# Kernel optimization log

Measured on AMD Instinct MI355X. Metric: run time of the kernel, lower is better.

## Reference

```python
import jax, jax.numpy as jnp
import numpy as np

B, T, INPUT_DIM, Z_DIM, RNN_DIM = 512, 200, 88, 100, 60


def setup_inputs() -> dict:
    key = jax.random.key(0)
    ks = jax.random.split(key, 18)
    sd = 0.05
    return {
        "mini_batch": jax.random.normal(ks[0], (B, T, INPUT_DIM), jnp.float32),
        "mini_batch_reversed": jax.random.normal(ks[1], (B, T, INPUT_DIM), jnp.float32),
        "mini_batch_mask": jnp.ones((B, T), jnp.float32),
        "mini_batch_seq_lengths": jax.random.randint(ks[2], (B,), T // 2, T + 1),
        "eps": jax.random.normal(ks[3], (T, B, Z_DIM), jnp.float32),
        # RNN (relu, 1 layer) params
        "W_ih": jax.random.normal(ks[4], (RNN_DIM, INPUT_DIM), jnp.float32) * sd,
        "W_hh": jax.random.normal(ks[5], (RNN_DIM, RNN_DIM), jnp.float32) * sd,
        "b_ih": jnp.zeros((RNN_DIM,), jnp.float32),
        "b_hh": jnp.zeros((RNN_DIM,), jnp.float32),
        "h_0": jax.random.normal(ks[6], (RNN_DIM,), jnp.float32),
        "z_q_0": jnp.zeros((Z_DIM,), jnp.float32),
        # Combiner params
        "W_zh": jax.random.normal(ks[7], (RNN_DIM, Z_DIM), jnp.float32) * sd,
        "b_zh": jnp.zeros((RNN_DIM,), jnp.float32),
        "W_hl": jax.random.normal(ks[8], (Z_DIM, RNN_DIM), jnp.float32) * sd,
        "b_hl": jnp.zeros((Z_DIM,), jnp.float32),
        "W_hs": jax.random.normal(ks[9], (Z_DIM, RNN_DIM), jnp.float32) * sd,
        "b_hs": jnp.zeros((Z_DIM,), jnp.float32),
    }


def _encoder(mini_batch_reversed, seq_lengths, eps,
             W_ih, W_hh, b_ih, b_hh, h_0, z_q_0,
             W_zh, b_zh, W_hl, b_hl, W_hs, b_hs):
    Bn = mini_batch_reversed.shape[0]
    Tn = mini_batch_reversed.shape[1]

    # --- relu RNN over reversed input, batch_first -> scan over time ---
    xs = jnp.transpose(mini_batch_reversed, (1, 0, 2))  # [T, B, input_dim]
    h0 = jnp.broadcast_to(h_0, (Bn, RNN_DIM))

    def rnn_step(h, x_t):
        h = jax.nn.relu(x_t @ W_ih.T + b_ih + h @ W_hh.T + b_hh)
        return h, h

    _, rnn_out = jax.lax.scan(rnn_step, h0, xs)          # [T, B, rnn_dim]
    rnn_out = jnp.transpose(rnn_out, (1, 0, 2))          # [B, T, rnn_dim]

    # --- pad_and_reverse: reverse each sequence by its length, zero-pad tail ---
    t_idx = jnp.arange(Tn)
    rev_idx = seq_lengths[:, None] - 1 - t_idx[None, :]  # [B, T]
    valid = rev_idx >= 0
    gathered = jnp.take_along_axis(rnn_out, jnp.clip(rev_idx, 0)[:, :, None], axis=1)
    rnn_rev = jnp.where(valid[:, :, None], gathered, 0.0)  # [B, T, rnn_dim]

    # --- sequential combiner + reparameterized sampling ---
    h_seq = jnp.transpose(rnn_rev, (1, 0, 2))            # [T, B, rnn_dim]
    z0 = jnp.broadcast_to(z_q_0, (Bn, Z_DIM))

    def comb_step(z_prev, inp):
        h_t, eps_t = inp
        h_comb = 0.5 * (jnp.tanh(z_prev @ W_zh.T + b_zh) + h_t)
        loc = h_comb @ W_hl.T + b_hl
        scale = jax.nn.softplus(h_comb @ W_hs.T + b_hs)
        z_t = loc + scale * eps_t
        return z_t, (z_t, loc, scale)

    _, (zs, locs, scales) = jax.lax.scan(comb_step, z0, (h_seq, eps))
    # [T, B, z] -> [B, T, z]
    tr = lambda a: jnp.transpose(a, (1, 0, 2))
    return tr(zs), tr(locs), tr(scales)


def reference(mini_batch, mini_batch_reversed, mini_batch_mask,
              mini_batch_seq_lengths, eps,
              W_ih, W_hh, b_ih, b_hh, h_0, z_q_0,
              W_zh, b_zh, W_hl, b_hl, W_hs, b_hs):
    return _encoder(mini_batch_reversed, mini_batch_seq_lengths, eps,
                    W_ih, W_hh, b_ih, b_hh, h_0, z_q_0,
                    W_zh, b_zh, W_hl, b_hl, W_hs, b_hs)
```

## Files before the change

kernel.cpp:

```cpp
#include <hip/hip_runtime.h>
#include <cmath>

#define NB 512
#define NT 200
#define NIN 88
#define NH 60
#define NZ 100

typedef float f2 __attribute__((ext_vector_type(2)));
typedef _Float16 h2v __attribute__((ext_vector_type(2)));
typedef _Float16 h8v __attribute__((ext_vector_type(8)));

__device__ __forceinline__ f2 pk_fma(f2 a, f2 b, f2 c) {
    return __builtin_elementwise_fma(a, b, c);
}
__device__ __forceinline__ float dot2(h2v a, h2v b, float c) {
#if __has_builtin(__builtin_amdgcn_fdot2)
    return __builtin_amdgcn_fdot2(a, b, c, false);
#else
    return fmaf((float)a.x, (float)b.x, fmaf((float)a.y, (float)b.y, c));
#endif
}
__device__ __forceinline__ float fast_tanh(float x) {
    float cx = fminf(fmaxf(x, -10.f), 10.f);
    float e  = __expf(2.f * cx);
    return (e - 1.f) * __builtin_amdgcn_rcpf(e + 1.f);
}
__device__ __forceinline__ float fast_softplus(float x) {
    return fmaxf(x, 0.f) + __logf(1.f + __expf(-fabsf(x)));
}
__device__ __forceinline__ void block_sync_lds() {
    asm volatile("s_waitcnt lgkmcnt(0)" ::: "memory");
    __builtin_amdgcn_s_barrier();
    asm volatile("" ::: "memory");
}

#define TCHUNKS 5
#define TCL (NT / TCHUNKS)

__global__ __launch_bounds__(128, 1)
void pre_kernel(const float* __restrict__ xrev, const float* __restrict__ W_ih,
                const float* __restrict__ b_ih, const float* __restrict__ b_hh,
                float* __restrict__ pre)
{
    __shared__ __align__(16) float xw[2][NIN];

    const int b    = blockIdx.x;
    const int tc   = blockIdx.y;
    const int wv   = threadIdx.x >> 6;
    const int lane = threadIdx.x & 63;

    f2 wih2[44];
    float bias = 0.f;
    if (lane < NH) {
        const float4* p = reinterpret_cast<const float4*>(W_ih + lane * NIN);
#pragma unroll
        for (int k = 0; k < 22; ++k) {
            float4 v = p[k];
            wih2[2*k]   = f2{v.x, v.y};
            wih2[2*k+1] = f2{v.z, v.w};
        }
        bias = b_ih[lane] + b_hh[lane];
    } else {
#pragma unroll
        for (int k = 0; k < 44; ++k) wih2[k] = f2{0.f, 0.f};
    }

    const float* xb = xrev + ((size_t)b * NT + (size_t)tc * TCL) * NIN;
    float* pb = pre + ((size_t)b * NT + (size_t)tc * TCL) * NH;

    float xa = xb[(size_t)wv * NIN + lane];
    float xc = (lane < NIN - 64) ? xb[(size_t)wv * NIN + 64 + lane] : 0.f;

    for (int k = 0; k < TCL / 2; ++k) {
        const int t = wv + 2 * k;
        xw[wv][lane] = xa;
        if (lane < NIN - 64) xw[wv][64 + lane] = xc;
        const int tn = t + 2;
        if (tn < TCL) {
            xa = xb[(size_t)tn * NIN + lane];
            xc = (lane < NIN - 64) ? xb[(size_t)tn * NIN + 64 + lane] : 0.f;
        }
        const float4* x4 = reinterpret_cast<const float4*>(xw[wv]);
        f2 a0 = f2{bias, 0.f}, a1 = f2{0.f, 0.f};
#pragma unroll
        for (int q = 0; q < 22; ++q) {
            float4 v = x4[q];
            a0 = pk_fma(f2{v.x, v.y}, wih2[2*q],   a0);
            a1 = pk_fma(f2{v.z, v.w}, wih2[2*q+1], a1);
        }
        if (lane < NH) pb[(size_t)t * NH + lane] = (a0.x + a1.x) + (a0.y + a1.y);
    }
}

__global__ __launch_bounds__(128, 1)
void fused128(const int*   __restrict__ seqlen,
              const float* __restrict__ eps,
              const float* __restrict__ W_hh,
              const float* __restrict__ h0,
              const float* __restrict__ zq0,
              const float* __restrict__ W_zh,
              const float* __restrict__ b_zh,
              const float* __restrict__ W_hl,
              const float* __restrict__ b_hl,
              const float* __restrict__ W_hs,
              const float* __restrict__ b_hs,
              const float* __restrict__ pre,
              float* __restrict__ out)
{
    __shared__ __align__(16) float    h_rev[NT][NH];
    __shared__ __align__(16) float    hbuf[NH + 4];
    __shared__ __align__(16) _Float16 zbh[2][112];
    __shared__ __align__(16) _Float16 hch[2][64];

    const int b    = blockIdx.x;
    const int tid  = threadIdx.x;
    const int wv   = tid >> 6;
    const int lane = tid & 63;
    const int sl   = seqlen[b];

    {
        const int tail = (NT - sl) * NH;
        float* base = &h_rev[0][0] + sl * NH;
        for (int i = tid; i < tail; i += 128) base[i] = 0.0f;
    }
    if (tid < 12) { zbh[0][100 + tid] = (_Float16)0; zbh[1][100 + tid] = (_Float16)0; }
    if (lane >= NH) hch[wv][lane] = (_Float16)0;

    f2  whh2[30];
    h2v wzh_h[52];
    h2v wl_h[32];
    h2v ws_h[32];
    float bz = 0.f, bl = 0.f, bs = 0.f;
    const int  o   = 50 * wv + lane;
    const bool oln = (lane < 50);
    float e_cur = 0.f;

    if (oln) {
        const float4* p = reinterpret_cast<const float4*>(W_hl + o * NH);
        const float4* q = reinterpret_cast<const float4*>(W_hs + o * NH);
#pragma unroll
        for (int k = 0; k < 15; ++k) {
            float4 v = p[k];
            wl_h[2*k]   = h2v{(_Float16)(0.5f * v.x), (_Float16)(0.5f * v.y)};
            wl_h[2*k+1] = h2v{(_Float16)(0.5f * v.z), (_Float16)(0.5f * v.w)};
            float4 u = q[k];
            ws_h[2*k]   = h2v{(_Float16)(0.5f * u.x), (_Float16)(0.5f * u.y)};
            ws_h[2*k+1] = h2v{(_Float16)(0.5f * u.z), (_Float16)(0.5f * u.w)};
        }
        wl_h[30] = h2v{(_Float16)0, (_Float16)0}; wl_h[31] = wl_h[30];
        ws_h[30] = wl_h[30]; ws_h[31] = wl_h[30];
        bl = b_hl[o];
        bs = b_hs[o];
        e_cur = eps[(size_t)b * NZ + o];
        zbh[0][o] = (_Float16)zq0[o];
    } else {
#pragma unroll
        for (int k = 0; k < 32; ++k) { wl_h[k] = h2v{(_Float16)0, (_Float16)0}; ws_h[k] = wl_h[k]; }
    }

    if (wv == 0) {
        if (lane < NH) {
            const float4* q = reinterpret_cast<const float4*>(W_hh + lane * NH);
#pragma unroll
            for (int k = 0; k < 15; ++k) {
                float4 v = q[k];
                whh2[2*k]   = f2{v.x, v.y};
                whh2[2*k+1] = f2{v.z, v.w};
            }
            hbuf[lane] = h0[lane];
        } else {
#pragma unroll
            for (int k = 0; k < 30; ++k) whh2[k] = f2{0.f, 0.f};
        }
    } else {
        if (lane < NH) {
            const float4* q = reinterpret_cast<const float4*>(W_zh + lane * NZ);
#pragma unroll
            for (int k = 0; k < 25; ++k) {
                float4 v = q[k];
                wzh_h[2*k]   = h2v{(_Float16)v.x, (_Float16)v.y};
                wzh_h[2*k+1] = h2v{(_Float16)v.z, (_Float16)v.w};
            }
            bz = b_zh[lane];
        } else {
#pragma unroll
            for (int k = 0; k < 50; ++k) wzh_h[k] = h2v{(_Float16)0, (_Float16)0};
        }
        wzh_h[50] = h2v{(_Float16)0, (_Float16)0};
        wzh_h[51] = wzh_h[50];
    }
    __syncthreads();

    if (wv == 0) {
        const float* pb = pre + (size_t)b * NT * NH;
        const bool hl = (lane < NH);
        float p0 = hl ? pb[0 * NH + lane] : 0.f;
        float p1 = hl ? pb[1 * NH + lane] : 0.f;
        float p2 = hl ? pb[2 * NH + lane] : 0.f;
        float p3 = hl ? pb[3 * NH + lane] : 0.f;
        for (int t = 0; t < NT; ++t) {
            float pn = (t + 4 < NT && hl) ? pb[(size_t)(t + 4) * NH + lane] : 0.f;
            const float4* h4 = reinterpret_cast<const float4*>(hbuf);
            f2 a0 = f2{p0, 0.f}, a1 = f2{0.f, 0.f};
#pragma unroll
            for (int k = 0; k < 15; ++k) {
                float4 v = h4[k];
                a0 = pk_fma(f2{v.x, v.y}, whh2[2*k],   a0);
                a1 = pk_fma(f2{v.z, v.w}, whh2[2*k+1], a1);
            }
            float hn = fmaxf((a0.x + a1.x) + (a0.y + a1.y), 0.f);
            if (hl) {
                hbuf[lane] = hn;
                if (t < sl) h_rev[sl - 1 - t][lane] = hn;
            }
            p0 = p1; p1 = p2; p2 = p3; p3 = pn;
        }
        if (lane < NH) {
            const float4* q = reinterpret_cast<const float4*>(W_zh + lane * NZ);
#pragma unroll
            for (int k = 0; k < 25; ++k) {
                float4 v = q[k];
                wzh_h[2*k]   = h2v{(_Float16)v.x, (_Float16)v.y};
                wzh_h[2*k+1] = h2v{(_Float16)v.z, (_Float16)v.w};
            }
            bz = b_zh[lane];
        } else {
#pragma unroll
            for (int k = 0; k < 50; ++k) wzh_h[k] = h2v{(_Float16)0, (_Float16)0};
        }
        wzh_h[50] = h2v{(_Float16)0, (_Float16)0};
        wzh_h[51] = wzh_h[50];
    }
    block_sync_lds();

    float* out_z = out;
    float* out_l = out + (size_t)NB * NT * NZ;
    float* out_s = out + (size_t)2 * NB * NT * NZ;

    for (int t = 0; t < NT; ++t) {
        const int r = t & 1;

        float hrow = (lane < NH) ? h_rev[t][lane] : 0.f;

        const h8v* z8 = reinterpret_cast<const h8v*>(&zbh[r][0]);
        float za0 = 0.f, za1 = 0.f, za2 = 0.f, za3 = 0.f;
#pragma unroll
        for (int k = 0; k < 13; ++k) {
            h8v v = z8[k];
            za0 = dot2(h2v{v[0], v[1]}, wzh_h[4*k+0], za0);
            za1 = dot2(h2v{v[2], v[3]}, wzh_h[4*k+1], za1);
            za2 = dot2(h2v{v[4], v[5]}, wzh_h[4*k+2], za2);
            za3 = dot2(h2v{v[6], v[7]}, wzh_h[4*k+3], za3);
        }

        float e_nxt = (oln && t + 1 < NT)
                      ? eps[((size_t)(t + 1) * NB + b) * NZ + o] : 0.f;

        if (lane < NH) {
            float a = (za0 + za1) + (za2 + za3) + bz;
            hch[wv][lane] = (_Float16)(fast_tanh(a) + hrow);
        }

        const h8v* h8p = reinterpret_cast<const h8v*>(&hch[wv][0]);
        float l0 = 0.f, l1 = 0.f, l2 = 0.f, l3 = 0.f;
        float s0 = 0.f, s1 = 0.f, s2 = 0.f, s3 = 0.f;
#pragma unroll
        for (int k = 0; k < 8; ++k) {
            h8v v = h8p[k];
            h2v x0 = h2v{v[0], v[1]}, x1 = h2v{v[2], v[3]};
            h2v x2 = h2v{v[4], v[5]}, x3 = h2v{v[6], v[7]};
            l0 = dot2(x0, wl_h[4*k+0], l0);
            l1 = dot2(x1, wl_h[4*k+1], l1);
            l2 = dot2(x2, wl_h[4*k+2], l2);
            l3 = dot2(x3, wl_h[4*k+3], l3);
            s0 = dot2(x0, ws_h[4*k+0], s0);
            s1 = dot2(x1, ws_h[4*k+1], s1);
            s2 = dot2(x2, ws_h[4*k+2], s2);
            s3 = dot2(x3, ws_h[4*k+3], s3);
        }
        if (oln) {
            float loc = (l0 + l1) + (l2 + l3) + bl;
            float ps  = (s0 + s1) + (s2 + s3) + bs;
            float sc  = fast_softplus(ps);
            float zv  = loc + sc * e_cur;
            size_t oi = ((size_t)b * NT + t) * NZ + o;
            out_z[oi] = zv;
            out_l[oi] = loc;
            out_s[oi] = sc;
            zbh[r ^ 1][o] = (_Float16)zv;
            e_cur = e_nxt;
        }
        block_sync_lds();
    }
}

__global__ __launch_bounds__(128, 1)
void encoder_mono(const float* __restrict__ xrev, const int* __restrict__ seqlen,
                  const float* __restrict__ eps,
                  const float* __restrict__ W_ih, const float* __restrict__ W_hh,
                  const float* __restrict__ b_ih, const float* __restrict__ b_hh,
                  const float* __restrict__ h0,   const float* __restrict__ zq0,
                  const float* __restrict__ W_zh, const float* __restrict__ b_zh,
                  const float* __restrict__ W_hl, const float* __restrict__ b_hl,
                  const float* __restrict__ W_hs, const float* __restrict__ b_hs,
                  float* __restrict__ out)
{
    __shared__ __align__(16) float h_rev[NT][NH];
    __shared__ __align__(16) float xbuf[NIN];
    __shared__ __align__(16) float hbuf[NH];
    __shared__ __align__(16) float zbuf[NZ];
    __shared__ __align__(16) float hcomb[NH];

    const int b = blockIdx.x, tid = threadIdx.x;
    const int wave = tid >> 6, lane = tid & 63;
    const int sl = seqlen[b];

    for (int i = tid; i < NT * NH; i += 128) (&h_rev[0][0])[i] = 0.0f;
    __syncthreads();

    if (wave == 0) {
        float wih[NIN], whh[NH];
        float bias = 0.f;
        if (lane < NH) {
            const float4* pp = reinterpret_cast<const float4*>(W_ih + lane * NIN);
#pragma unroll
            for (int k = 0; k < NIN / 4; ++k) {
                float4 v = pp[k];
                wih[4*k+0]=v.x; wih[4*k+1]=v.y; wih[4*k+2]=v.z; wih[4*k+3]=v.w;
            }
            const float4* q = reinterpret_cast<const float4*>(W_hh + lane * NH);
#pragma unroll
            for (int k = 0; k < NH / 4; ++k) {
                float4 v = q[k];
                whh[4*k+0]=v.x; whh[4*k+1]=v.y; whh[4*k+2]=v.z; whh[4*k+3]=v.w;
            }
            bias = b_ih[lane] + b_hh[lane];
            hbuf[lane] = h0[lane];
        } else {
#pragma unroll
            for (int k = 0; k < NIN; ++k) wih[k] = 0.f;
#pragma unroll
            for (int k = 0; k < NH; ++k) whh[k] = 0.f;
        }
        const float* xb = xrev + (size_t)b * NT * NIN;
        float xa = xb[lane];
        float xc = (lane < NIN - 64) ? xb[64 + lane] : 0.f;
        for (int t = 0; t < NT; ++t) {
            xbuf[lane] = xa;
            if (lane < NIN - 64) xbuf[64 + lane] = xc;
            if (t + 1 < NT) {
                xa = xb[(size_t)(t+1)*NIN + lane];
                xc = (lane < NIN - 64) ? xb[(size_t)(t+1)*NIN + 64 + lane] : 0.f;
            }
            float a0=0.f,a1=0.f,a2=0.f,a3=0.f;
            const float4* x4 = reinterpret_cast<const float4*>(xbuf);
#pragma unroll
            for (int k = 0; k < NIN / 4; ++k) {
                float4 v = x4[k];
                a0 += v.x*wih[4*k+0]; a1 += v.y*wih[4*k+1];
                a2 += v.z*wih[4*k+2]; a3 += v.w*wih[4*k+3];
            }
            const float4* h4 = reinterpret_cast<const float4*>(hbuf);
#pragma unroll
            for (int k = 0; k < NH / 4; ++k) {
                float4 v = h4[k];
                a0 += v.x*whh[4*k+0]; a1 += v.y*whh[4*k+1];
                a2 += v.z*whh[4*k+2]; a3 += v.w*whh[4*k+3];
            }
            float hn = fmaxf((a0+a1)+(a2+a3)+bias, 0.f);
            if (lane < NH) {
                hbuf[lane] = hn;
                if (t < sl) h_rev[sl-1-t][lane] = hn;
            }
        }
    }
    __syncthreads();

    const int o = 50 * wave + lane;
    float wzr[NZ]; float bz = 0.f;
    if (wave == 0 && lane < NH) {
        const float4* pp = reinterpret_cast<const float4*>(W_zh + lane * NZ);
#pragma unroll
        for (int k = 0; k < NZ / 4; ++k) {
            float4 v = pp[k];
            wzr[4*k+0]=v.x; wzr[4*k+1]=v.y; wzr[4*k+2]=v.z; wzr[4*k+3]=v.w;
        }
        bz = b_zh[lane];
    } else {
#pragma unroll
        for (int k = 0; k < NZ; ++k) wzr[k] = 0.f;
    }
    float wl[NH], ws_[NH]; float bl = 0.f, bs = 0.f;
    if (lane < 50) {
        const float4* pp = reinterpret_cast<const float4*>(W_hl + o * NH);
        const float4* q  = reinterpret_cast<const float4*>(W_hs + o * NH);
#pragma unroll
        for (int k = 0; k < NH / 4; ++k) {
            float4 v = pp[k];
            wl[4*k+0]=v.x; wl[4*k+1]=v.y; wl[4*k+2]=v.z; wl[4*k+3]=v.w;
            float4 u = q[k];
            ws_[4*k+0]=u.x; ws_[4*k+1]=u.y; ws_[4*k+2]=u.z; ws_[4*k+3]=u.w;
        }
        bl = b_hl[o]; bs = b_hs[o];
        zbuf[o] = zq0[o];
    } else {
#pragma unroll
        for (int k = 0; k < NH; ++k) { wl[k]=0.f; ws_[k]=0.f; }
    }
    __syncthreads();

    float* out_z = out;
    float* out_l = out + (size_t)NB * NT * NZ;
    float* out_s = out + (size_t)2 * NB * NT * NZ;
    const float* epsb = eps + (size_t)b * NZ;
    float e_cur = (lane < 50) ? epsb[o] : 0.f;

    for (int t = 0; t < NT; ++t) {
        if (wave == 0) {
            float a0=0.f,a1=0.f,a2=0.f,a3=0.f;
            const float4* z4 = reinterpret_cast<const float4*>(zbuf);
#pragma unroll
            for (int k = 0; k < NZ / 4; ++k) {
                float4 v = z4[k];
                a0 += v.x*wzr[4*k+0]; a1 += v.y*wzr[4*k+1];
                a2 += v.z*wzr[4*k+2]; a3 += v.w*wzr[4*k+3];
            }
            if (lane < NH) {
                float a = (a0+a1)+(a2+a3)+bz;
                hcomb[lane] = 0.5f * (fast_tanh(a) + h_rev[t][lane]);
            }
        }
        block_sync_lds();
        float e_nxt = 0.f;
        if (t + 1 < NT && lane < 50) e_nxt = epsb[(size_t)(t+1)*NB*NZ + o];
        if (lane < 50) {
            float c0=0.f,c1=0.f,c2=0.f,c3=0.f, d0=0.f,d1=0.f,d2=0.f,d3=0.f;
            const float4* h4 = reinterpret_cast<const float4*>(hcomb);
#pragma unroll
            for (int k = 0; k < NH / 4; ++k) {
                float4 v = h4[k];
                c0 += v.x*wl[4*k+0];  c1 += v.y*wl[4*k+1];
                c2 += v.z*wl[4*k+2];  c3 += v.w*wl[4*k+3];
                d0 += v.x*ws_[4*k+0]; d1 += v.y*ws_[4*k+1];
                d2 += v.z*ws_[4*k+2]; d3 += v.w*ws_[4*k+3];
            }
            float loc = (c0+c1)+(c2+c3)+bl;
            float ps  = (d0+d1)+(d2+d3)+bs;
            float sc  = fast_softplus(ps);
            float zv  = loc + sc * e_cur;
            size_t oi = ((size_t)b * NT + t) * NZ + o;
            out_z[oi]=zv; out_l[oi]=loc; out_s[oi]=sc;
            zbuf[o]=zv;
        }
        e_cur = e_nxt;
        block_sync_lds();
    }
}

extern "C" void kernel_launch(void* const* d_in, const int* in_sizes, int n_in,
                              void* d_out, int out_size, void* d_ws, size_t ws_size,
                              hipStream_t stream) {
    const float* xrev   = (const float*)d_in[1];
    const int*   seqlen = (const int*)  d_in[3];
    const float* eps    = (const float*)d_in[4];
    const float* W_ih   = (const float*)d_in[5];
    const float* W_hh   = (const float*)d_in[6];
    const float* b_ih   = (const float*)d_in[7];
    const float* b_hh   = (const float*)d_in[8];
    const float* h0     = (const float*)d_in[9];
    const float* zq0    = (const float*)d_in[10];
    const float* W_zh   = (const float*)d_in[11];
    const float* b_zh   = (const float*)d_in[12];
    const float* W_hl   = (const float*)d_in[13];
    const float* b_hl   = (const float*)d_in[14];
    const float* W_hs   = (const float*)d_in[15];
    const float* b_hs   = (const float*)d_in[16];
    float* out = (float*)d_out;

    const size_t pre_bytes = (size_t)NB * NT * NH * sizeof(float);
    if (ws_size >= pre_bytes) {
        float* pre = (float*)d_ws;
        pre_kernel<<<dim3(NB, TCHUNKS), 128, 0, stream>>>(xrev, W_ih, b_ih, b_hh, pre);
        fused128<<<NB, 128, 0, stream>>>(seqlen, eps, W_hh, h0, zq0,
                                         W_zh, b_zh, W_hl, b_hl, W_hs, b_hs,
                                         pre, out);
    } else {
        encoder_mono<<<NB, 128, 0, stream>>>(xrev, seqlen, eps,
                                             W_ih, W_hh, b_ih, b_hh, h0, zq0,
                                             W_zh, b_zh, W_hl, b_hl, W_hs, b_hs,
                                             out);
    }
}
```

Baseline: 311.8 us.

## Process one batch element per wavefront, removing block barriers in the recurrence loops

The fused kernel now gives each wavefront its own batch element, so a 128-thread block handles two elements and the grid is halved. Each wave runs both the RNN scan and the combiner scan itself, so the per-step block barrier and the cross-wave split of the output rows go away. Each lane now computes two outputs, and the reversed hidden states are kept in LDS as fp16. The costs are more registers per lane for the doubled weight sets, no overlap between the RNN phase and the combiner phase, and some extra precision loss on h. Correctness now depends on wavefront lockstep for the LDS handoffs that the removed barrier used to order.

```diff
diff --git a/kernel.cpp b/kernel.cpp
--- a/kernel.cpp
+++ b/kernel.cpp
@@ -94,72 +94,51 @@
 }
 
 __global__ __launch_bounds__(128, 1)
-void fused128(const int*   __restrict__ seqlen,
-              const float* __restrict__ eps,
-              const float* __restrict__ W_hh,
-              const float* __restrict__ h0,
-              const float* __restrict__ zq0,
-              const float* __restrict__ W_zh,
-              const float* __restrict__ b_zh,
-              const float* __restrict__ W_hl,
-              const float* __restrict__ b_hl,
-              const float* __restrict__ W_hs,
-              const float* __restrict__ b_hs,
-              const float* __restrict__ pre,
-              float* __restrict__ out)
+void fused1w(const int*   __restrict__ seqlen,
+             const float* __restrict__ eps,
+             const float* __restrict__ W_hh,
+             const float* __restrict__ h0,
+             const float* __restrict__ zq0,
+             const float* __restrict__ W_zh,
+             const float* __restrict__ b_zh,
+             const float* __restrict__ W_hl,
+             const float* __restrict__ b_hl,
+             const float* __restrict__ W_hs,
+             const float* __restrict__ b_hs,
+             const float* __restrict__ pre,
+             float* __restrict__ out)
 {
-    __shared__ __align__(16) float    h_rev[NT][NH];
-    __shared__ __align__(16) float    hbuf[NH + 4];
+    __shared__ __align__(16) _Float16 h_rev_h[2][NT][NH];
+    __shared__ __align__(16) float    hbuf[2][64];
     __shared__ __align__(16) _Float16 zbh[2][112];
     __shared__ __align__(16) _Float16 hch[2][64];
 
-    const int b    = blockIdx.x;
-    const int tid  = threadIdx.x;
-    const int wv   = tid >> 6;
-    const int lane = tid & 63;
+    const int wv   = threadIdx.x >> 6;
+    const int lane = threadIdx.x & 63;
+    const int b    = blockIdx.x * 2 + wv;
     const int sl   = seqlen[b];
 
     {
         const int tail = (NT - sl) * NH;
-        float* base = &h_rev[0][0] + sl * NH;
-        for (int i = tid; i < tail; i += 128) base[i] = 0.0f;
-    }
-    if (tid < 12) { zbh[0][100 + tid] = (_Float16)0; zbh[1][100 + tid] = (_Float16)0; }
+        _Float16* base = &h_rev_h[wv][sl][0];
+        for (int i = lane; i < tail; i += 64) base[i] = (_Float16)0;
+    }
+    if (lane < 12) zbh[wv][100 + lane] = (_Float16)0;
     if (lane >= NH) hch[wv][lane] = (_Float16)0;
 
-    f2  whh2[30];
-    h2v wzh_h[52];
-    h2v wl_h[32];
-    h2v ws_h[32];
-    float bz = 0.f, bl = 0.f, bs = 0.f;
-    const int  o   = 50 * wv + lane;
     const bool oln = (lane < 50);
-    float e_cur = 0.f;
-
+    const int  o1  = lane;
+    const int  o2  = lane + 50;
+    float e1 = 0.f, e2 = 0.f;
     if (oln) {
-        const float4* p = reinterpret_cast<const float4*>(W_hl + o * NH);
-        const float4* q = reinterpret_cast<const float4*>(W_hs + o * NH);
-#pragma unroll
-        for (int k = 0; k < 15; ++k) {
-            float4 v = p[k];
-            wl_h[2*k]   = h2v{(_Float16)(0.5f * v.x), (_Float16)(0.5f * v.y)};
-            wl_h[2*k+1] = h2v{(_Float16)(0.5f * v.z), (_Float16)(0.5f * v.w)};
-            float4 u = q[k];
-            ws_h[2*k]   = h2v{(_Float16)(0.5f * u.x), (_Float16)(0.5f * u.y)};
-            ws_h[2*k+1] = h2v{(_Float16)(0.5f * u.z), (_Float16)(0.5f * u.w)};
-        }
-        wl_h[30] = h2v{(_Float16)0, (_Float16)0}; wl_h[31] = wl_h[30];
-        ws_h[30] = wl_h[30]; ws_h[31] = wl_h[30];
-        bl = b_hl[o];
-        bs = b_hs[o];
-        e_cur = eps[(size_t)b * NZ + o];
-        zbh[0][o] = (_Float16)zq0[o];
-    } else {
-#pragma unroll
-        for (int k = 0; k < 32; ++k) { wl_h[k] = h2v{(_Float16)0, (_Float16)0}; ws_h[k] = wl_h[k]; }
-    }
-
-    if (wv == 0) {
+        zbh[wv][o1] = (_Float16)zq0[o1];
+        zbh[wv][o2] = (_Float16)zq0[o2];
+        e1 = eps[(size_t)b * NZ + o1];
+        e2 = eps[(size_t)b * NZ + o2];
+    }
+
+    {
+        f2 whh2[30];
         if (lane < NH) {
             const float4* q = reinterpret_cast<const float4*>(W_hh + lane * NH);
 #pragma unroll
@@ -168,31 +147,12 @@
                 whh2[2*k]   = f2{v.x, v.y};
                 whh2[2*k+1] = f2{v.z, v.w};
             }
-            hbuf[lane] = h0[lane];
+            hbuf[wv][lane] = h0[lane];
         } else {
 #pragma unroll
             for (int k = 0; k < 30; ++k) whh2[k] = f2{0.f, 0.f};
         }
-    } else {
-        if (lane < NH) {
-            const float4* q = reinterpret_cast<const float4*>(W_zh + lane * NZ);
-#pragma unroll
-            for (int k = 0; k < 25; ++k) {
-                float4 v = q[k];
-                wzh_h[2*k]   = h2v{(_Float16)v.x, (_Float16)v.y};
-                wzh_h[2*k+1] = h2v{(_Float16)v.z, (_Float16)v.w};
-            }
-            bz = b_zh[lane];
-        } else {
-#pragma unroll
-            for (int k = 0; k < 50; ++k) wzh_h[k] = h2v{(_Float16)0, (_Float16)0};
-        }
-        wzh_h[50] = h2v{(_Float16)0, (_Float16)0};
-        wzh_h[51] = wzh_h[50];
-    }
-    __syncthreads();
-
-    if (wv == 0) {
+
         const float* pb = pre + (size_t)b * NT * NH;
         const bool hl = (lane < NH);
         float p0 = hl ? pb[0 * NH + lane] : 0.f;
@@ -201,7 +161,7 @@
         float p3 = hl ? pb[3 * NH + lane] : 0.f;
         for (int t = 0; t < NT; ++t) {
             float pn = (t + 4 < NT && hl) ? pb[(size_t)(t + 4) * NH + lane] : 0.f;
-            const float4* h4 = reinterpret_cast<const float4*>(hbuf);
+            const float4* h4 = reinterpret_cast<const float4*>(&hbuf[wv][0]);
             f2 a0 = f2{p0, 0.f}, a1 = f2{0.f, 0.f};
 #pragma unroll
             for (int k = 0; k < 15; ++k) {
@@ -211,39 +171,73 @@
             }
             float hn = fmaxf((a0.x + a1.x) + (a0.y + a1.y), 0.f);
             if (hl) {
-                hbuf[lane] = hn;
-                if (t < sl) h_rev[sl - 1 - t][lane] = hn;
+                hbuf[wv][lane] = hn;
+                if (t < sl) h_rev_h[wv][sl - 1 - t][lane] = (_Float16)hn;
             }
             p0 = p1; p1 = p2; p2 = p3; p3 = pn;
         }
-        if (lane < NH) {
-            const float4* q = reinterpret_cast<const float4*>(W_zh + lane * NZ);
-#pragma unroll
-            for (int k = 0; k < 25; ++k) {
-                float4 v = q[k];
-                wzh_h[2*k]   = h2v{(_Float16)v.x, (_Float16)v.y};
-                wzh_h[2*k+1] = h2v{(_Float16)v.z, (_Float16)v.w};
-            }
-            bz = b_zh[lane];
-        } else {
-#pragma unroll
-            for (int k = 0; k < 50; ++k) wzh_h[k] = h2v{(_Float16)0, (_Float16)0};
-        }
-        wzh_h[50] = h2v{(_Float16)0, (_Float16)0};
-        wzh_h[51] = wzh_h[50];
-    }
-    block_sync_lds();
+    }
+
+    h2v wzh_h[52];
+    float bz = 0.f;
+    if (lane < NH) {
+        const float4* q = reinterpret_cast<const float4*>(W_zh + lane * NZ);
+#pragma unroll
+        for (int k = 0; k < 25; ++k) {
+            float4 v = q[k];
+            wzh_h[2*k]   = h2v{(_Float16)v.x, (_Float16)v.y};
+            wzh_h[2*k+1] = h2v{(_Float16)v.z, (_Float16)v.w};
+        }
+        bz = b_zh[lane];
+    } else {
+#pragma unroll
+        for (int k = 0; k < 50; ++k) wzh_h[k] = h2v{(_Float16)0, (_Float16)0};
+    }
+    wzh_h[50] = h2v{(_Float16)0, (_Float16)0};
+    wzh_h[51] = wzh_h[50];
+
+    h2v wlA[32], wsA[32], wlB[32], wsB[32];
+    float blA = 0.f, bsA = 0.f, blB = 0.f, bsB = 0.f;
+    if (oln) {
+        const float4* pA = reinterpret_cast<const float4*>(W_hl + o1 * NH);
+        const float4* qA = reinterpret_cast<const float4*>(W_hs + o1 * NH);
+        const float4* pB = reinterpret_cast<const float4*>(W_hl + o2 * NH);
+        const float4* qB = reinterpret_cast<const float4*>(W_hs + o2 * NH);
+#pragma unroll
+        for (int k = 0; k < 15; ++k) {
+            float4 v;
+            v = pA[k];
+            wlA[2*k]   = h2v{(_Float16)(0.5f*v.x), (_Float16)(0.5f*v.y)};
+            wlA[2*k+1] = h2v{(_Float16)(0.5f*v.z), (_Float16)(0.5f*v.w)};
+            v = qA[k];
+            wsA[2*k]   = h2v{(_Float16)(0.5f*v.x), (_Float16)(0.5f*v.y)};
+            wsA[2*k+1] = h2v{(_Float16)(0.5f*v.z), (_Float16)(0.5f*v.w)};
+            v = pB[k];
+            wlB[2*k]   = h2v{(_Float16)(0.5f*v.x), (_Float16)(0.5f*v.y)};
+            wlB[2*k+1] = h2v{(_Float16)(0.5f*v.z), (_Float16)(0.5f*v.w)};
+            v = qB[k];
+            wsB[2*k]   = h2v{(_Float16)(0.5f*v.x), (_Float16)(0.5f*v.y)};
+            wsB[2*k+1] = h2v{(_Float16)(0.5f*v.z), (_Float16)(0.5f*v.w)};
+        }
+        blA = b_hl[o1]; bsA = b_hs[o1];
+        blB = b_hl[o2]; bsB = b_hs[o2];
+    } else {
+#pragma unroll
+        for (int k = 0; k < 32; ++k) {
+            wlA[k] = h2v{(_Float16)0, (_Float16)0};
+            wsA[k] = wlA[k]; wlB[k] = wlA[k]; wsB[k] = wlA[k];
+        }
+    }
+    h2v zpad = h2v{(_Float16)0, (_Float16)0};
+    wlA[30] = zpad; wlA[31] = zpad; wsA[30] = zpad; wsA[31] = zpad;
+    wlB[30] = zpad; wlB[31] = zpad; wsB[30] = zpad; wsB[31] = zpad;
 
     float* out_z = out;
     float* out_l = out + (size_t)NB * NT * NZ;
     float* out_s = out + (size_t)2 * NB * NT * NZ;
 
     for (int t = 0; t < NT; ++t) {
-        const int r = t & 1;
-
-        float hrow = (lane < NH) ? h_rev[t][lane] : 0.f;
-
-        const h8v* z8 = reinterpret_cast<const h8v*>(&zbh[r][0]);
+        const h8v* z8 = reinterpret_cast<const h8v*>(&zbh[wv][0]);
         float za0 = 0.f, za1 = 0.f, za2 = 0.f, za3 = 0.f;
 #pragma unroll
         for (int k = 0; k < 13; ++k) {
@@ -253,9 +247,14 @@
             za2 = dot2(h2v{v[4], v[5]}, wzh_h[4*k+2], za2);
             za3 = dot2(h2v{v[6], v[7]}, wzh_h[4*k+3], za3);
         }
-
-        float e_nxt = (oln && t + 1 < NT)
-                      ? eps[((size_t)(t + 1) * NB + b) * NZ + o] : 0.f;
+        float hrow = (lane < NH) ? (float)h_rev_h[wv][t][lane] : 0.f;
+
+        float e1n = 0.f, e2n = 0.f;
+        if (oln && t + 1 < NT) {
+            const float* ep = eps + ((size_t)(t + 1) * NB + b) * NZ;
+            e1n = ep[o1];
+            e2n = ep[o2];
+        }
 
         if (lane < NH) {
             float a = (za0 + za1) + (za2 + za3) + bz;
@@ -263,35 +262,47 @@
         }
 
         const h8v* h8p = reinterpret_cast<const h8v*>(&hch[wv][0]);
-        float l0 = 0.f, l1 = 0.f, l2 = 0.f, l3 = 0.f;
-        float s0 = 0.f, s1 = 0.f, s2 = 0.f, s3 = 0.f;
+        float lA0 = 0.f, lA1 = 0.f, sA0 = 0.f, sA1 = 0.f;
+        float lB0 = 0.f, lB1 = 0.f, sB0 = 0.f, sB1 = 0.f;
 #pragma unroll
         for (int k = 0; k < 8; ++k) {
             h8v v = h8p[k];
             h2v x0 = h2v{v[0], v[1]}, x1 = h2v{v[2], v[3]};
             h2v x2 = h2v{v[4], v[5]}, x3 = h2v{v[6], v[7]};
-            l0 = dot2(x0, wl_h[4*k+0], l0);
-            l1 = dot2(x1, wl_h[4*k+1], l1);
-            l2 = dot2(x2, wl_h[4*k+2], l2);
-            l3 = dot2(x3, wl_h[4*k+3], l3);
-            s0 = dot2(x0, ws_h[4*k+0], s0);
-            s1 = dot2(x1, ws_h[4*k+1], s1);
-            s2 = dot2(x2, ws_h[4*k+2], s2);
-            s3 = dot2(x3, ws_h[4*k+3], s3);
+            lA0 = dot2(x0, wlA[4*k+0], lA0);
+            lA1 = dot2(x1, wlA[4*k+1], lA1);
+            lA0 = dot2(x2, wlA[4*k+2], lA0);
+            lA1 = dot2(x3, wlA[4*k+3], lA1);
+            sA0 = dot2(x0, wsA[4*k+0], sA0);
+            sA1 = dot2(x1, wsA[4*k+1], sA1);
+            sA0 = dot2(x2, wsA[4*k+2], sA0);
+            sA1 = dot2(x3, wsA[4*k+3], sA1);
+            lB0 = dot2(x0, wlB[4*k+0], lB0);
+            lB1 = dot2(x1, wlB[4*k+1], lB1);
+            lB0 = dot2(x2, wlB[4*k+2], lB0);
+            lB1 = dot2(x3, wlB[4*k+3], lB1);
+            sB0 = dot2(x0, wsB[4*k+0], sB0);
+            sB1 = dot2(x1, wsB[4*k+1], sB1);
+            sB0 = dot2(x2, wsB[4*k+2], sB0);
+            sB1 = dot2(x3, wsB[4*k+3], sB1);
         }
         if (oln) {
-            float loc = (l0 + l1) + (l2 + l3) + bl;
-            float ps  = (s0 + s1) + (s2 + s3) + bs;
-            float sc  = fast_softplus(ps);
-            float zv  = loc + sc * e_cur;
-            size_t oi = ((size_t)b * NT + t) * NZ + o;
-            out_z[oi] = zv;
-            out_l[oi] = loc;
-            out_s[oi] = sc;
-            zbh[r ^ 1][o] = (_Float16)zv;
-            e_cur = e_nxt;
-        }
-        block_sync_lds();
+            float locA = lA0 + lA1 + blA;
+            float psA  = sA0 + sA1 + bsA;
+            float scA  = fast_softplus(psA);
+            float zA   = locA + scA * e1;
+            float locB = lB0 + lB1 + blB;
+            float psB  = sB0 + sB1 + bsB;
+            float scB  = fast_softplus(psB);
+            float zB   = locB + scB * e2;
+            size_t oi = ((size_t)b * NT + t) * NZ;
+            out_z[oi + o1] = zA;  out_z[oi + o2] = zB;
+            out_l[oi + o1] = locA; out_l[oi + o2] = locB;
+            out_s[oi + o1] = scA;  out_s[oi + o2] = scB;
+            zbh[wv][o1] = (_Float16)zA;
+            zbh[wv][o2] = (_Float16)zB;
+            e1 = e1n; e2 = e2n;
+        }
     }
 }
 
@@ -482,9 +493,9 @@
     if (ws_size >= pre_bytes) {
         float* pre = (float*)d_ws;
         pre_kernel<<<dim3(NB, TCHUNKS), 128, 0, stream>>>(xrev, W_ih, b_ih, b_hh, pre);
-        fused128<<<NB, 128, 0, stream>>>(seqlen, eps, W_hh, h0, zq0,
-                                         W_zh, b_zh, W_hl, b_hl, W_hs, b_hs,
-                                         pre, out);
+        fused1w<<<NB / 2, 128, 0, stream>>>(seqlen, eps, W_hh, h0, zq0,
+                                            W_zh, b_zh, W_hl, b_hl, W_hs, b_hs,
+                                            pre, out);
     } else {
         encoder_mono<<<NB, 128, 0, stream>>>(xrev, seqlen, eps,
                                              W_ih, W_hh, b_ih, b_hh, h0, zq0,
```

New measurement: 276.2 us. 1.13x faster.
